# Performance work log

Measured on AMD Instinct MI355X. Metric: run time of the kernel, lower is better.

Reference implementation:

```python
import jax, jax.numpy as jnp
import numpy as np

NUM_HEADS = 16

def setup_inputs() -> dict:
    key = jax.random.key(0)
    ks = jax.random.split(key, 6)
    B, S, D = 2, 2048, 1024
    x = jax.random.normal(ks[0], (B, S, D), dtype=jnp.float32)
    s = 1.0 / np.sqrt(D)
    Wq = jax.random.normal(ks[1], (D, D), dtype=jnp.float32) * s
    Wk = jax.random.normal(ks[2], (D, D), dtype=jnp.float32) * s
    Wv = jax.random.normal(ks[3], (D, D), dtype=jnp.float32) * s
    Wff = jax.random.normal(ks[4], (D, D), dtype=jnp.float32) * s
    bff = jax.random.normal(ks[5], (D,), dtype=jnp.float32) * 0.01
    return {"x": x, "Wq": Wq, "Wk": Wk, "Wv": Wv, "Wff": Wff, "bff": bff}

def reference(x, Wq, Wk, Wv, Wff, bff):
    B, S, D = x.shape
    H = NUM_HEADS
    Dh = D // H
    # Q/K/V projections (bias-free Linears). Original scales Q by 1/sqrt(hidden_size).
    q = (x @ Wq.T) * (1.0 / jnp.sqrt(jnp.asarray(D, x.dtype)))
    k = x @ Wk.T
    v = x @ Wv.T
    q = q.reshape(B, S, H, Dh)
    k = k.reshape(B, S, H, Dh)
    v = v.reshape(B, S, H, Dh)
    # Blockwise online-softmax attention is mathematically identical to
    # full softmax attention over all keys (no causal mask in source).
    scores = jnp.einsum('bqhd,bkhd->bhqk', q, k)
    attn = jax.nn.softmax(scores, axis=-1)
    out = jnp.einsum('bhqk,bkhd->bqhd', attn, v).reshape(B, S, D)
    # Final feedforward Linear(hidden, hidden) with bias.
    return out @ Wff.T + bff
```

## Files before the change

### kernel.cpp

```cpp
#include <hip/hip_runtime.h>
#include <stdint.h>

typedef __attribute__((ext_vector_type(8))) short bf16x8;
typedef __attribute__((ext_vector_type(4))) float f32x4;

__device__ __forceinline__ uint16_t f2bf(float f) {
  union { float f; uint32_t u; } a; a.f = f;
  uint32_t u = a.u;
  u += 0x7FFFu + ((u >> 16) & 1u);
  return (uint16_t)(u >> 16);
}

__device__ __forceinline__ uint32_t pk_bf16(float a, float b) {
#if __has_builtin(__builtin_amdgcn_cvt_pk_bf16_f32)
  auto r = __builtin_amdgcn_cvt_pk_bf16_f32(a, b);
  uint32_t u; __builtin_memcpy(&u, &r, sizeof(u));
  return u;
#else
  return (uint32_t)f2bf(a) | ((uint32_t)f2bf(b) << 16);
#endif
}

__device__ __forceinline__ void gld_lds16(const uint16_t* g, uint16_t* l) {
  __builtin_amdgcn_global_load_lds(
      (const __attribute__((address_space(1))) void*)g,
      (__attribute__((address_space(3))) void*)l, 16, 0, 0);
}

__global__ void cast_all(const float* __restrict__ x, const float* __restrict__ wq,
                         const float* __restrict__ wk, const float* __restrict__ wv,
                         const float* __restrict__ wff,
                         uint16_t* __restrict__ xb, uint16_t* __restrict__ wqb,
                         uint16_t* __restrict__ wkb, uint16_t* __restrict__ wvb,
                         uint16_t* __restrict__ wffb) {
  int i = blockIdx.x * blockDim.x + threadIdx.x;
  const float* src; uint16_t* dst; int off;
  if (i < 1048576)      { src = x;   dst = xb;   off = i; }
  else if (i < 1310720) { src = wq;  dst = wqb;  off = i - 1048576; }
  else if (i < 1572864) { src = wk;  dst = wkb;  off = i - 1310720; }
  else if (i < 1835008) { src = wv;  dst = wvb;  off = i - 1572864; }
  else                  { src = wff; dst = wffb; off = i - 1835008; }
  float4 v = ((const float4*)src)[off];
  uint2 o; o.x = pk_bf16(v.x, v.y); o.y = pk_bf16(v.z, v.w);
  ((uint2*)dst)[off] = o;
}

__device__ __forceinline__ void gemm_tile(const uint16_t* __restrict__ Abase,
                                          const uint16_t* __restrict__ Bbase,
                                          uint16_t* lds, f32x4 acc[4][4]) {
  const int tid  = threadIdx.x;
  const int w    = tid >> 6;
  const int lane = tid & 63;
  const int wm   = w >> 1, wn = w & 1;
  const int lrow = lane & 15;
  const int quad = lane >> 4;
  const int srow = lane >> 3;
  const int lc   = (lane & 7) ^ srow;
  const int sx   = lrow & 7;
  uint16_t* a_lds = lds;
  uint16_t* b_lds = lds + 8192;

#pragma unroll
  for (int mt = 0; mt < 4; ++mt)
#pragma unroll
    for (int nt = 0; nt < 4; ++nt)
      acc[mt][nt] = (f32x4){0.f, 0.f, 0.f, 0.f};

  const uint16_t* ag = Abase + (size_t)(w * 32 + srow) * 1024 + lc * 8;
  const uint16_t* bg = Bbase + (size_t)(w * 32 + srow) * 1024 + lc * 8;

  for (int k0 = 0; k0 < 1024; k0 += 64) {
#pragma unroll
    for (int i8 = 0; i8 < 4; ++i8) {
      gld_lds16(ag + (size_t)i8 * 8 * 1024 + k0, a_lds + (w * 4 + i8) * 512);
      gld_lds16(bg + (size_t)i8 * 8 * 1024 + k0, b_lds + (w * 4 + i8) * 512);
    }
    __syncthreads();
#pragma unroll
    for (int ks = 0; ks < 2; ++ks) {
      bf16x8 af[4], bfr[4];
      const int c = ((ks * 4 + quad) ^ sx) << 3;
#pragma unroll
      for (int mt = 0; mt < 4; ++mt)
        af[mt] = *(const bf16x8*)(a_lds + (wm * 64 + mt * 16 + lrow) * 64 + c);
#pragma unroll
      for (int nt = 0; nt < 4; ++nt)
        bfr[nt] = *(const bf16x8*)(b_lds + (wn * 64 + nt * 16 + lrow) * 64 + c);
#pragma unroll
      for (int mt = 0; mt < 4; ++mt)
#pragma unroll
        for (int nt = 0; nt < 4; ++nt)
          acc[mt][nt] = __builtin_amdgcn_mfma_f32_16x16x32_bf16(af[mt], bfr[nt], acc[mt][nt], 0, 0, 0);
    }
    __syncthreads();
  }
}

__global__ __launch_bounds__(256) void gemm_qkv(
    const uint16_t* __restrict__ x,
    const uint16_t* __restrict__ wq, const uint16_t* __restrict__ wk, const uint16_t* __restrict__ wv,
    uint16_t* __restrict__ qo, uint16_t* __restrict__ ko, uint16_t* __restrict__ vto) {
  __shared__ __align__(16) uint16_t lds[16384];
  const int m0 = blockIdx.x * 128, n0 = blockIdx.y * 128, z = blockIdx.z;
  f32x4 acc[4][4];
  if (z < 2) {
    const uint16_t* W = (z == 0) ? wq : wk;
    gemm_tile(W + (size_t)n0 * 1024, x + (size_t)m0 * 1024, lds, acc);
  } else {
    gemm_tile(x + (size_t)m0 * 1024, wv + (size_t)n0 * 1024, lds, acc);
  }

  const int lane = threadIdx.x & 63, w = threadIdx.x >> 6;
  const int wm = w >> 1, wn = w & 1, lrow = lane & 15, quad = lane >> 4;
  const float scale = (z == 0) ? 0.045084222f : 1.0f;

  if (z < 2) {
    uint16_t* outp = (z == 0) ? qo : ko;
#pragma unroll
    for (int mt = 0; mt < 4; ++mt)
#pragma unroll
      for (int nt = 0; nt < 4; ++nt) {
        int i0 = wm * 64 + mt * 16 + quad * 4;
        int j  = wn * 64 + nt * 16 + lrow;
        int n = n0 + i0, m = m0 + j;
        int b = m >> 11, s = m & 2047, h = n >> 6, dh = n & 63;
        uint2 dd;
        dd.x = pk_bf16(acc[mt][nt][0] * scale, acc[mt][nt][1] * scale);
        dd.y = pk_bf16(acc[mt][nt][2] * scale, acc[mt][nt][3] * scale);
        *(uint2*)(outp + ((size_t)((b * 16 + h) * 2048 + s)) * 64 + dh) = dd;
      }
  } else {
#pragma unroll
    for (int mt = 0; mt < 4; ++mt)
#pragma unroll
      for (int nt = 0; nt < 4; ++nt) {
        int i0 = wm * 64 + mt * 16 + quad * 4;
        int j  = wn * 64 + nt * 16 + lrow;
        int mg = m0 + i0, n = n0 + j;
        int b = mg >> 11, s0 = mg & 2047, h = n >> 6, dh = n & 63;
        uint2 dd;
        dd.x = pk_bf16(acc[mt][nt][0], acc[mt][nt][1]);
        dd.y = pk_bf16(acc[mt][nt][2], acc[mt][nt][3]);
        *(uint2*)(vto + ((size_t)((b * 16 + h) * 64 + dh)) * 2048 + s0) = dd;
      }
  }
}

__global__ __launch_bounds__(256) void gemm_ff(
    const uint16_t* __restrict__ ao, const uint16_t* __restrict__ wff,
    const float* __restrict__ bff, float* __restrict__ out) {
  __shared__ __align__(16) uint16_t lds[16384];
  const int m0 = blockIdx.x * 128, n0 = blockIdx.y * 128;
  f32x4 acc[4][4];
  gemm_tile(wff + (size_t)n0 * 1024, ao + (size_t)m0 * 1024, lds, acc);

  const int lane = threadIdx.x & 63, w = threadIdx.x >> 6;
  const int wm = w >> 1, wn = w & 1, lrow = lane & 15, quad = lane >> 4;
#pragma unroll
  for (int mt = 0; mt < 4; ++mt) {
    int i0 = wm * 64 + mt * 16 + quad * 4;
    int n = n0 + i0;
    float4 bias = *(const float4*)(bff + n);
#pragma unroll
    for (int nt = 0; nt < 4; ++nt) {
      int m = m0 + wn * 64 + nt * 16 + lrow;
      float4 vv;
      vv.x = acc[mt][nt][0] + bias.x; vv.y = acc[mt][nt][1] + bias.y;
      vv.z = acc[mt][nt][2] + bias.z; vv.w = acc[mt][nt][3] + bias.w;
      *(float4*)(out + (size_t)m * 1024 + n) = vv;
    }
  }
}

__global__ __launch_bounds__(256, 2) void attn(
    const uint16_t* __restrict__ q, const uint16_t* __restrict__ k,
    const uint16_t* __restrict__ vt, uint16_t* __restrict__ ao) {
  __shared__ __align__(16) uint16_t k_lds[2][4096];
  __shared__ __align__(16) uint16_t v_lds[2][4096];
  __shared__ __align__(16) uint16_t p_lds[4][2048];
  const int tid = threadIdx.x, w = tid >> 6, lane = tid & 63;
  const int lrow = lane & 15, quad = lane >> 4;
  const int srow = lane >> 3, lc = (lane & 7) ^ srow, sx = lrow & 7;
  const int bh = blockIdx.y, qb = blockIdx.x;
  const uint16_t* Q = q  + (size_t)bh * (2048 * 64);
  const uint16_t* K = k  + (size_t)bh * (2048 * 64);
  const uint16_t* V = vt + (size_t)bh * (64 * 2048);
  uint16_t* pw = p_lds[w];
  const int cswz = (lrow & 7) << 1;

  const int qr0 = qb * 128 + w * 32;
  bf16x8 qf[2][2];
#pragma unroll
  for (int qh = 0; qh < 2; ++qh)
#pragma unroll
    for (int ks = 0; ks < 2; ++ks)
      qf[qh][ks] = *(const bf16x8*)(Q + (size_t)(qr0 + qh * 16 + lrow) * 64 + ks * 32 + quad * 8);

  f32x4 o[2][4];
#pragma unroll
  for (int qh = 0; qh < 2; ++qh)
#pragma unroll
    for (int dt = 0; dt < 4; ++dt) o[qh][dt] = (f32x4){0.f, 0.f, 0.f, 0.f};
  float ls[2] = {0.f, 0.f};

  auto stage = [&](int kb, int bi) {
#pragma unroll
    for (int i2 = 0; i2 < 2; ++i2) {
      int i8 = w * 2 + i2;
      gld_lds16(K + (size_t)(kb * 64 + i8 * 8 + srow) * 64 + lc * 8, &k_lds[bi][i8 * 512]);
      gld_lds16(V + (size_t)(i8 * 8 + srow) * 2048 + kb * 64 + lc * 8, &v_lds[bi][i8 * 512]);
    }
  };
  stage(0, 0);

  for (int kb = 0; kb < 32; ++kb) {
    const int bi = kb & 1;
    __syncthreads();
    if (kb + 1 < 32) stage(kb + 1, bi ^ 1);

    f32x4 s[2][4];
#pragma unroll
    for (int qh = 0; qh < 2; ++qh)
#pragma unroll
      for (int kt = 0; kt < 4; ++kt) s[qh][kt] = (f32x4){0.f, 0.f, 0.f, 0.f};
#pragma unroll
    for (int ks = 0; ks < 2; ++ks) {
      const int c = ((ks * 4 + quad) ^ sx) << 3;
#pragma unroll
      for (int kt = 0; kt < 4; ++kt) {
        bf16x8 kf = *(const bf16x8*)(&k_lds[bi][(kt * 16 + lrow) * 64 + c]);
        s[0][kt] = __builtin_amdgcn_mfma_f32_16x16x32_bf16(kf, qf[0][ks], s[0][kt], 0, 0, 0);
        s[1][kt] = __builtin_amdgcn_mfma_f32_16x16x32_bf16(kf, qf[1][ks], s[1][kt], 0, 0, 0);
      }
    }

#pragma unroll
    for (int qh = 0; qh < 2; ++qh)
#pragma unroll
      for (int kt = 0; kt < 4; ++kt) {
        float p0 = exp2f(s[qh][kt][0]);
        float p1 = exp2f(s[qh][kt][1]);
        float p2 = exp2f(s[qh][kt][2]);
        float p3 = exp2f(s[qh][kt][3]);
        ls[qh] += (p0 + p1) + (p2 + p3);
        uint2 dd; dd.x = pk_bf16(p0, p1); dd.y = pk_bf16(p2, p3);
        *(uint2*)(pw + (qh * 16 + lrow) * 64 + (((kt * 4 + quad) ^ cswz) << 2)) = dd;
      }

#pragma unroll
    for (int ks = 0; ks < 2; ++ks) {
      bf16x8 pa0 = *(const bf16x8*)(pw + lrow * 64 + (((ks * 8 + quad * 2) ^ cswz) << 2));
      bf16x8 pa1 = *(const bf16x8*)(pw + (16 + lrow) * 64 + (((ks * 8 + quad * 2) ^ cswz) << 2));
      const int c = ((ks * 4 + quad) ^ sx) << 3;
#pragma unroll
      for (int dt = 0; dt < 4; ++dt) {
        bf16x8 vf = *(const bf16x8*)(&v_lds[bi][(dt * 16 + lrow) * 64 + c]);
        o[0][dt] = __builtin_amdgcn_mfma_f32_16x16x32_bf16(vf, pa0, o[0][dt], 0, 0, 0);
        o[1][dt] = __builtin_amdgcn_mfma_f32_16x16x32_bf16(vf, pa1, o[1][dt], 0, 0, 0);
      }
    }
  }

  const int b = bh >> 4, h = bh & 15;
#pragma unroll
  for (int qh = 0; qh < 2; ++qh) {
    float l = ls[qh];
    l += __shfl_xor(l, 16);
    l += __shfl_xor(l, 32);
    float inv = 1.0f / l;
    int sg = qr0 + qh * 16 + lrow;
#pragma unroll
    for (int dt = 0; dt < 4; ++dt) {
      uint2 dd;
      dd.x = pk_bf16(o[qh][dt][0] * inv, o[qh][dt][1] * inv);
      dd.y = pk_bf16(o[qh][dt][2] * inv, o[qh][dt][3] * inv);
      *(uint2*)(ao + (size_t)(b * 2048 + sg) * 1024 + h * 64 + dt * 16 + quad * 4) = dd;
    }
  }
}

extern "C" void kernel_launch(void* const* d_in, const int* in_sizes, int n_in,
                              void* d_out, int out_size, void* d_ws, size_t ws_size,
                              hipStream_t stream) {
  const float* x   = (const float*)d_in[0];
  const float* Wq  = (const float*)d_in[1];
  const float* Wk  = (const float*)d_in[2];
  const float* Wv  = (const float*)d_in[3];
  const float* Wff = (const float*)d_in[4];
  const float* bff = (const float*)d_in[5];
  float* out = (float*)d_out;

  uint16_t* ws = (uint16_t*)d_ws;
  uint16_t* x_bf   = ws;
  uint16_t* wq_bf  = ws + 4194304;
  uint16_t* wk_bf  = ws + 5242880;
  uint16_t* wv_bf  = ws + 6291456;
  uint16_t* wff_bf = ws + 7340032;
  uint16_t* q_bf   = ws + 8388608;
  uint16_t* k_bf   = ws + 12582912;
  uint16_t* vt_bf  = ws + 16777216;
  uint16_t* ao_bf  = ws + 20971520;

  cast_all<<<8192, 256, 0, stream>>>(x, Wq, Wk, Wv, Wff, x_bf, wq_bf, wk_bf, wv_bf, wff_bf);

  gemm_qkv<<<dim3(32, 8, 3), 256, 0, stream>>>(x_bf, wq_bf, wk_bf, wv_bf, q_bf, k_bf, vt_bf);
  attn<<<dim3(16, 32), 256, 0, stream>>>(q_bf, k_bf, vt_bf, ao_bf);
  gemm_ff<<<dim3(32, 8), 256, 0, stream>>>(ao_bf, wff_bf, bff, out);
}
```

Before: 215.5 us.

## Stage GEMM epilogues through LDS for coalesced stores; use fast exp2 in attention

The QKV and FF GEMM epilogues now write accumulators into padded LDS and then issue row-contiguous 16-byte global stores, replacing the scattered 8-byte and strided per-fragment stores. The transposed V output now gets coalesced writes along the sequence dimension. The attention softmax switches to the hardware exp2 intrinsic and a truncating bf16 pack fallback when the packed-convert builtin is missing. This adds LDS traffic and barriers in the epilogue, and raises LDS use from 32 KB to 34 KB per block, which could affect occupancy.

Result: faster. 190.8 us (-11.5%).

```diff
diff --git a/kernel.cpp b/kernel.cpp
--- a/kernel.cpp
+++ b/kernel.cpp
@@ -18,6 +18,26 @@
   return u;
 #else
   return (uint32_t)f2bf(a) | ((uint32_t)f2bf(b) << 16);
+#endif
+}
+
+__device__ __forceinline__ uint32_t pk_bf16_fast(float a, float b) {
+#if __has_builtin(__builtin_amdgcn_cvt_pk_bf16_f32)
+  auto r = __builtin_amdgcn_cvt_pk_bf16_f32(a, b);
+  uint32_t u; __builtin_memcpy(&u, &r, sizeof(u));
+  return u;
+#else
+  uint32_t ua, ub;
+  __builtin_memcpy(&ua, &a, 4); __builtin_memcpy(&ub, &b, 4);
+  return __builtin_amdgcn_perm(ub, ua, 0x07060302u);
+#endif
+}
+
+__device__ __forceinline__ float fast_exp2(float x) {
+#if __has_builtin(__builtin_amdgcn_exp2f)
+  return __builtin_amdgcn_exp2f(x);
+#else
+  return exp2f(x);
 #endif
 }
 
@@ -100,7 +120,7 @@
     const uint16_t* __restrict__ x,
     const uint16_t* __restrict__ wq, const uint16_t* __restrict__ wk, const uint16_t* __restrict__ wv,
     uint16_t* __restrict__ qo, uint16_t* __restrict__ ko, uint16_t* __restrict__ vto) {
-  __shared__ __align__(16) uint16_t lds[16384];
+  __shared__ __align__(16) uint16_t lds[17408];
   const int m0 = blockIdx.x * 128, n0 = blockIdx.y * 128, z = blockIdx.z;
   f32x4 acc[4][4];
   if (z < 2) {
@@ -110,65 +130,85 @@
     gemm_tile(x + (size_t)m0 * 1024, wv + (size_t)n0 * 1024, lds, acc);
   }
 
-  const int lane = threadIdx.x & 63, w = threadIdx.x >> 6;
+  const int tid = threadIdx.x;
+  const int lane = tid & 63, w = tid >> 6;
   const int wm = w >> 1, wn = w & 1, lrow = lane & 15, quad = lane >> 4;
   const float scale = (z == 0) ? 0.045084222f : 1.0f;
 
+#pragma unroll
+  for (int mt = 0; mt < 4; ++mt)
+#pragma unroll
+    for (int nt = 0; nt < 4; ++nt) {
+      int i0 = wm * 64 + mt * 16 + quad * 4;
+      int j  = wn * 64 + nt * 16 + lrow;
+      uint2 dd;
+      dd.x = pk_bf16(acc[mt][nt][0] * scale, acc[mt][nt][1] * scale);
+      dd.y = pk_bf16(acc[mt][nt][2] * scale, acc[mt][nt][3] * scale);
+      *(uint2*)(&lds[j * 136 + i0]) = dd;
+    }
+  __syncthreads();
+
+  uint16_t* outp = (z == 0) ? qo : (z == 1) ? ko : vto;
   if (z < 2) {
-    uint16_t* outp = (z == 0) ? qo : ko;
-#pragma unroll
-    for (int mt = 0; mt < 4; ++mt)
-#pragma unroll
-      for (int nt = 0; nt < 4; ++nt) {
-        int i0 = wm * 64 + mt * 16 + quad * 4;
-        int j  = wn * 64 + nt * 16 + lrow;
-        int n = n0 + i0, m = m0 + j;
-        int b = m >> 11, s = m & 2047, h = n >> 6, dh = n & 63;
-        uint2 dd;
-        dd.x = pk_bf16(acc[mt][nt][0] * scale, acc[mt][nt][1] * scale);
-        dd.y = pk_bf16(acc[mt][nt][2] * scale, acc[mt][nt][3] * scale);
-        *(uint2*)(outp + ((size_t)((b * 16 + h) * 2048 + s)) * 64 + dh) = dd;
-      }
+#pragma unroll
+    for (int it = 0; it < 8; ++it) {
+      int idx = it * 256 + tid;
+      int jj = idx >> 4, cc = idx & 15;
+      uint4 v = *(const uint4*)(&lds[jj * 136 + cc * 8]);
+      int m = m0 + jj, n = n0 + cc * 8;
+      int b = m >> 11, s = m & 2047, h = n >> 6, dh = n & 63;
+      *(uint4*)(outp + ((size_t)((b * 16 + h) * 2048 + s)) * 64 + dh) = v;
+    }
   } else {
-#pragma unroll
-    for (int mt = 0; mt < 4; ++mt)
-#pragma unroll
-      for (int nt = 0; nt < 4; ++nt) {
-        int i0 = wm * 64 + mt * 16 + quad * 4;
-        int j  = wn * 64 + nt * 16 + lrow;
-        int mg = m0 + i0, n = n0 + j;
-        int b = mg >> 11, s0 = mg & 2047, h = n >> 6, dh = n & 63;
-        uint2 dd;
-        dd.x = pk_bf16(acc[mt][nt][0], acc[mt][nt][1]);
-        dd.y = pk_bf16(acc[mt][nt][2], acc[mt][nt][3]);
-        *(uint2*)(vto + ((size_t)((b * 16 + h) * 64 + dh)) * 2048 + s0) = dd;
-      }
+    int b = m0 >> 11, sbase = m0 & 2047;
+#pragma unroll
+    for (int it = 0; it < 8; ++it) {
+      int idx = it * 256 + tid;
+      int ff = idx >> 4, cc = idx & 15;
+      uint4 v = *(const uint4*)(&lds[ff * 136 + cc * 8]);
+      int n = n0 + ff, h = n >> 6, dh = n & 63;
+      *(uint4*)(outp + ((size_t)((b * 16 + h) * 64 + dh)) * 2048 + sbase + cc * 8) = v;
+    }
   }
 }
 
 __global__ __launch_bounds__(256) void gemm_ff(
     const uint16_t* __restrict__ ao, const uint16_t* __restrict__ wff,
     const float* __restrict__ bff, float* __restrict__ out) {
-  __shared__ __align__(16) uint16_t lds[16384];
+  __shared__ __align__(16) uint16_t lds[17408];
   const int m0 = blockIdx.x * 128, n0 = blockIdx.y * 128;
   f32x4 acc[4][4];
   gemm_tile(wff + (size_t)n0 * 1024, ao + (size_t)m0 * 1024, lds, acc);
 
-  const int lane = threadIdx.x & 63, w = threadIdx.x >> 6;
+  const int tid = threadIdx.x;
+  const int lane = tid & 63, w = tid >> 6;
   const int wm = w >> 1, wn = w & 1, lrow = lane & 15, quad = lane >> 4;
-#pragma unroll
-  for (int mt = 0; mt < 4; ++mt) {
-    int i0 = wm * 64 + mt * 16 + quad * 4;
-    int n = n0 + i0;
-    float4 bias = *(const float4*)(bff + n);
-#pragma unroll
-    for (int nt = 0; nt < 4; ++nt) {
-      int m = m0 + wn * 64 + nt * 16 + lrow;
-      float4 vv;
-      vv.x = acc[mt][nt][0] + bias.x; vv.y = acc[mt][nt][1] + bias.y;
-      vv.z = acc[mt][nt][2] + bias.z; vv.w = acc[mt][nt][3] + bias.w;
-      *(float4*)(out + (size_t)m * 1024 + n) = vv;
-    }
+  float* fl = (float*)lds;
+
+#pragma unroll
+  for (int p = 0; p < 2; ++p) {
+    if (wm == p) {
+#pragma unroll
+      for (int mt = 0; mt < 4; ++mt)
+#pragma unroll
+        for (int nt = 0; nt < 4; ++nt) {
+          int i0 = mt * 16 + quad * 4;
+          int j  = wn * 64 + nt * 16 + lrow;
+          *(f32x4*)(&fl[j * 68 + i0]) = acc[mt][nt];
+        }
+    }
+    __syncthreads();
+#pragma unroll
+    for (int it = 0; it < 8; ++it) {
+      int idx = it * 256 + tid;
+      int jj = idx >> 4, cc = idx & 15;
+      f32x4 v = *(const f32x4*)(&fl[jj * 68 + cc * 4]);
+      int n = n0 + p * 64 + cc * 4;
+      f32x4 bias = *(const f32x4*)(bff + n);
+      f32x4 vv = v + bias;
+      *(f32x4*)(out + (size_t)(m0 + jj) * 1024 + n) = vv;
+    }
+    __syncthreads();
   }
 }
 
@@ -238,12 +278,12 @@
     for (int qh = 0; qh < 2; ++qh)
 #pragma unroll
       for (int kt = 0; kt < 4; ++kt) {
-        float p0 = exp2f(s[qh][kt][0]);
-        float p1 = exp2f(s[qh][kt][1]);
-        float p2 = exp2f(s[qh][kt][2]);
-        float p3 = exp2f(s[qh][kt][3]);
+        float p0 = fast_exp2(s[qh][kt][0]);
+        float p1 = fast_exp2(s[qh][kt][1]);
+        float p2 = fast_exp2(s[qh][kt][2]);
+        float p3 = fast_exp2(s[qh][kt][3]);
         ls[qh] += (p0 + p1) + (p2 + p3);
-        uint2 dd; dd.x = pk_bf16(p0, p1); dd.y = pk_bf16(p2, p3);
+        uint2 dd; dd.x = pk_bf16_fast(p0, p1); dd.y = pk_bf16_fast(p2, p3);
         *(uint2*)(pw + (qh * 16 + lrow) * 64 + (((kt * 4 + quad) ^ cswz) << 2)) = dd;
       }
 
```
